# Kernel optimization log

Hardware: AMD Instinct MI355X
Metric: run time of the kernel (lower is better)

The kernel has to match this reference:

```python
import jax, jax.numpy as jnp
import numpy as np

REST = 0.0
DECAY = 0.2
THRESHOLD = 0.3
BETA = 0.02
SG_WIDTH = 1.0  # rectangular surrogate-gradient window width


@jax.custom_vjp
def spike(v, thresh):
    # forward: hard threshold, y = (v > thresh)
    return (v > thresh).astype(v.dtype)


def _spike_fwd(v, thresh):
    return spike(v, thresh), (v, thresh)


def _spike_bwd(res, g):
    v, thresh = res
    # rectangular surrogate gradient w.r.t. v; threshold gets the negative
    sg = (jnp.abs(v - thresh) < (SG_WIDTH * 0.5)).astype(g.dtype) / SG_WIDTH
    gv = g * sg
    return (gv, -gv)


spike.defvjp(_spike_fwd, _spike_bwd)


def setup_inputs() -> dict:
    key = jax.random.key(0)
    k1, k2 = jax.random.split(key)
    T, B, N = 512, 64, 1024
    tx = jax.random.normal(k1, (T, B, N), dtype=jnp.float32)
    TE = jax.random.normal(k2, (N, T), dtype=jnp.float32) * 0.1  # learned temporal encoding
    return {"tx": tx, "TE": TE}


def reference(tx, TE):
    # tx: [T, B, N] time-major input; TE: [N, T] per-neuron temporal encoding
    T, B, N = tx.shape
    v0 = jnp.full((B, N), REST, tx.dtype)
    y0 = jnp.zeros((B, N), tx.dtype)
    th0 = jnp.full((B, N), THRESHOLD, tx.dtype)

    def step(carry, inp):
        v, y, th = carry
        x, te_t = inp  # x: [B, N], te_t: [N]
        th = th + v * te_t - (th - THRESHOLD) * BETA
        v = v * DECAY * (1.0 - y) + x
        y = spike(v, th)
        return (v, y, th), y

    _, ty = jax.lax.scan(step, (v0, y0, th0), (tx, TE.T))
    return ty  # [T, B, N] spike trains
```

## Files before the change

kernel.cpp:

```cpp
#include <hip/hip_runtime.h>


#define T_STEPS 512
#define BN      (64 * 1024)

#define NTL(i)  __builtin_nontemporal_load(txp + (size_t)(i) * BN)
#define LD4(i)  (*reinterpret_cast<const float4*>(tep + (i)))

#define PFX(r, base) \
  r##0 .x = NTL((base)+0);  r##0 .y = NTL((base)+1);  r##0 .z = NTL((base)+2);  r##0 .w = NTL((base)+3);  \
  r##1 .x = NTL((base)+4);  r##1 .y = NTL((base)+5);  r##1 .z = NTL((base)+6);  r##1 .w = NTL((base)+7);  \
  r##2 .x = NTL((base)+8);  r##2 .y = NTL((base)+9);  r##2 .z = NTL((base)+10); r##2 .w = NTL((base)+11); \
  r##3 .x = NTL((base)+12); r##3 .y = NTL((base)+13); r##3 .z = NTL((base)+14); r##3 .w = NTL((base)+15);

#define PFE(r, base) \
  r##0 = LD4((base)+0); r##1 = LD4((base)+4); r##2 = LD4((base)+8); r##3 = LD4((base)+12);

#define STEP1(xv, tv, tt) { \
  float A_ = v * (tv); float B_ = th + A_; float C_ = th - 0.3f; \
  float D_ = C_ * 0.02f; th = B_ - D_; \
  float E_ = v * 0.2f; float F_ = 1.0f - y; float G_ = E_ * F_; \
  v = G_ + (xv); y = (v > th) ? 1.0f : 0.0f; \
  __builtin_nontemporal_store(y, outp + (size_t)(tt) * BN); }

#define COMP(r, s, base) \
  STEP1(r##0 .x, s##0 .x, (base)+0)  STEP1(r##0 .y, s##0 .y, (base)+1)  \
  STEP1(r##0 .z, s##0 .z, (base)+2)  STEP1(r##0 .w, s##0 .w, (base)+3)  \
  STEP1(r##1 .x, s##1 .x, (base)+4)  STEP1(r##1 .y, s##1 .y, (base)+5)  \
  STEP1(r##1 .z, s##1 .z, (base)+6)  STEP1(r##1 .w, s##1 .w, (base)+7)  \
  STEP1(r##2 .x, s##2 .x, (base)+8)  STEP1(r##2 .y, s##2 .y, (base)+9)  \
  STEP1(r##2 .z, s##2 .z, (base)+10) STEP1(r##2 .w, s##2 .w, (base)+11) \
  STEP1(r##3 .x, s##3 .x, (base)+12) STEP1(r##3 .y, s##3 .y, (base)+13) \
  STEP1(r##3 .z, s##3 .z, (base)+14) STEP1(r##3 .w, s##3 .w, (base)+15)

#define PIN() __builtin_amdgcn_sched_barrier(0)

__global__ __launch_bounds__(256, 1) void telif_kernel(
    const float* __restrict__ tx, const float* __restrict__ TE,
    float* __restrict__ out)
{
#pragma clang fp contract(off)

    const int flat = blockIdx.x * 256 + threadIdx.x;
    const int n = flat & 1023;

    const float* txp  = tx + flat;
    const float* tep  = TE + n * T_STEPS;
    float*       outp = out + flat;

    float v = 0.0f, y = 0.0f, th = 0.3f;

    float4 a0, a1, a2, a3, e0, e1, e2, e3;
    float4 b0, b1, b2, b3, f0, f1, f2, f3;
    float4 c0, c1, c2, c3, g0, g1, g2, g3;
    float4 d0, d1, d2, d3, h0, h1, h2, h3;

    PFX(a, 0)  PFE(e, 0)
    PFX(b, 16) PFE(f, 16)
    PIN();

#pragma unroll 1
    for (int t = 0; t < 448; t += 64) {
        PFX(c, t + 32) PFE(g, t + 32)
        PFX(d, t + 48) PFE(h, t + 48)
        PIN();
        COMP(a, e, t)
        COMP(b, f, t + 16)
        PIN();
        PFX(a, t + 64) PFE(e, t + 64)
        PFX(b, t + 80) PFE(f, t + 80)
        PIN();
        COMP(c, g, t + 32)
        COMP(d, h, t + 48)
        PIN();
    }
    PFX(c, 480) PFE(g, 480)
    PFX(d, 496) PFE(h, 496)
    PIN();
    COMP(a, e, 448)
    COMP(b, f, 464)
    COMP(c, g, 480)
    COMP(d, h, 496)
}

extern "C" void kernel_launch(void* const* d_in, const int* in_sizes, int n_in,
                              void* d_out, int out_size, void* d_ws, size_t ws_size,
                              hipStream_t stream) {
    const float* tx = (const float*)d_in[0];
    const float* TE = (const float*)d_in[1];
    float* out = (float*)d_out;
    telif_kernel<<<BN / 256, 256, 0, stream>>>(tx, TE, out);
}
```

Before: 233.6 us.

## Process two neurons per thread with 64-bit vector loads and smaller blocks

Result: no change. 235.5 us (+0.8%).

```diff
diff --git a/kernel.cpp b/kernel.cpp
--- a/kernel.cpp
+++ b/kernel.cpp
@@ -4,56 +4,71 @@
 #define T_STEPS 512
 #define BN      (64 * 1024)
 
-#define NTL(i)  __builtin_nontemporal_load(txp + (size_t)(i) * BN)
-#define LD4(i)  (*reinterpret_cast<const float4*>(tep + (i)))
+typedef float v2f __attribute__((ext_vector_type(2)));
+typedef float v4f __attribute__((ext_vector_type(4)));
+
+#define NTL2(i) __builtin_nontemporal_load(reinterpret_cast<const v2f*>(txp + (size_t)(i) * BN))
+#define LDA(i)  (*reinterpret_cast<const v4f*>(tep0 + (i)))
+#define LDB(i)  (*reinterpret_cast<const v4f*>(tep1 + (i)))
+
+#define DECLC(r, s) \
+  v2f r##00, r##01, r##02, r##03, r##04, r##05, r##06, r##07, \
+      r##08, r##09, r##10, r##11, r##12, r##13, r##14, r##15; \
+  v4f s##0, s##1, s##2, s##3, s##4, s##5, s##6, s##7;
 
 #define PFX(r, base) \
-  r##0 .x = NTL((base)+0);  r##0 .y = NTL((base)+1);  r##0 .z = NTL((base)+2);  r##0 .w = NTL((base)+3);  \
-  r##1 .x = NTL((base)+4);  r##1 .y = NTL((base)+5);  r##1 .z = NTL((base)+6);  r##1 .w = NTL((base)+7);  \
-  r##2 .x = NTL((base)+8);  r##2 .y = NTL((base)+9);  r##2 .z = NTL((base)+10); r##2 .w = NTL((base)+11); \
-  r##3 .x = NTL((base)+12); r##3 .y = NTL((base)+13); r##3 .z = NTL((base)+14); r##3 .w = NTL((base)+15);
+  r##00 = NTL2((base)+0);  r##01 = NTL2((base)+1);  r##02 = NTL2((base)+2);  r##03 = NTL2((base)+3);  \
+  r##04 = NTL2((base)+4);  r##05 = NTL2((base)+5);  r##06 = NTL2((base)+6);  r##07 = NTL2((base)+7);  \
+  r##08 = NTL2((base)+8);  r##09 = NTL2((base)+9);  r##10 = NTL2((base)+10); r##11 = NTL2((base)+11); \
+  r##12 = NTL2((base)+12); r##13 = NTL2((base)+13); r##14 = NTL2((base)+14); r##15 = NTL2((base)+15);
 
-#define PFE(r, base) \
-  r##0 = LD4((base)+0); r##1 = LD4((base)+4); r##2 = LD4((base)+8); r##3 = LD4((base)+12);
+#define PFE(s, base) \
+  s##0 = LDA((base));    s##1 = LDA((base)+4);  s##2 = LDA((base)+8);  s##3 = LDA((base)+12); \
+  s##4 = LDB((base));    s##5 = LDB((base)+4);  s##6 = LDB((base)+8);  s##7 = LDB((base)+12);
 
-#define STEP1(xv, tv, tt) { \
-  float A_ = v * (tv); float B_ = th + A_; float C_ = th - 0.3f; \
-  float D_ = C_ * 0.02f; th = B_ - D_; \
-  float E_ = v * 0.2f; float F_ = 1.0f - y; float G_ = E_ * F_; \
-  v = G_ + (xv); y = (v > th) ? 1.0f : 0.0f; \
-  __builtin_nontemporal_store(y, outp + (size_t)(tt) * BN); }
+#define STEP2(xv, t0v, t1v, tt) { \
+  float A0_ = v0 * (t0v); float B0_ = th0 + A0_; float C0_ = th0 - 0.3f; \
+  float D0_ = C0_ * 0.02f; th0 = B0_ - D0_; \
+  float E0_ = v0 * 0.2f; float F0_ = 1.0f - y0; float G0_ = E0_ * F0_; \
+  v0 = G0_ + (xv).x; y0 = (v0 > th0) ? 1.0f : 0.0f; \
+  float A1_ = v1 * (t1v); float B1_ = th1 + A1_; float C1_ = th1 - 0.3f; \
+  float D1_ = C1_ * 0.02f; th1 = B1_ - D1_; \
+  float E1_ = v1 * 0.2f; float F1_ = 1.0f - y1; float G1_ = E1_ * F1_; \
+  v1 = G1_ + (xv).y; y1 = (v1 > th1) ? 1.0f : 0.0f; \
+  v2f Y_; Y_.x = y0; Y_.y = y1; \
+  __builtin_nontemporal_store(Y_, reinterpret_cast<v2f*>(outp + (size_t)(tt) * BN)); }
 
 #define COMP(r, s, base) \
-  STEP1(r##0 .x, s##0 .x, (base)+0)  STEP1(r##0 .y, s##0 .y, (base)+1)  \
-  STEP1(r##0 .z, s##0 .z, (base)+2)  STEP1(r##0 .w, s##0 .w, (base)+3)  \
-  STEP1(r##1 .x, s##1 .x, (base)+4)  STEP1(r##1 .y, s##1 .y, (base)+5)  \
-  STEP1(r##1 .z, s##1 .z, (base)+6)  STEP1(r##1 .w, s##1 .w, (base)+7)  \
-  STEP1(r##2 .x, s##2 .x, (base)+8)  STEP1(r##2 .y, s##2 .y, (base)+9)  \
-  STEP1(r##2 .z, s##2 .z, (base)+10) STEP1(r##2 .w, s##2 .w, (base)+11) \
-  STEP1(r##3 .x, s##3 .x, (base)+12) STEP1(r##3 .y, s##3 .y, (base)+13) \
-  STEP1(r##3 .z, s##3 .z, (base)+14) STEP1(r##3 .w, s##3 .w, (base)+15)
+  STEP2(r##00, s##0 .x, s##4 .x, (base)+0)  STEP2(r##01, s##0 .y, s##4 .y, (base)+1)  \
+  STEP2(r##02, s##0 .z, s##4 .z, (base)+2)  STEP2(r##03, s##0 .w, s##4 .w, (base)+3)  \
+  STEP2(r##04, s##1 .x, s##5 .x, (base)+4)  STEP2(r##05, s##1 .y, s##5 .y, (base)+5)  \
+  STEP2(r##06, s##1 .z, s##5 .z, (base)+6)  STEP2(r##07, s##1 .w, s##5 .w, (base)+7)  \
+  STEP2(r##08, s##2 .x, s##6 .x, (base)+8)  STEP2(r##09, s##2 .y, s##6 .y, (base)+9)  \
+  STEP2(r##10, s##2 .z, s##6 .z, (base)+10) STEP2(r##11, s##2 .w, s##6 .w, (base)+11) \
+  STEP2(r##12, s##3 .x, s##7 .x, (base)+12) STEP2(r##13, s##3 .y, s##7 .y, (base)+13) \
+  STEP2(r##14, s##3 .z, s##7 .z, (base)+14) STEP2(r##15, s##3 .w, s##7 .w, (base)+15)
 
 #define PIN() __builtin_amdgcn_sched_barrier(0)
 
-__global__ __launch_bounds__(256, 1) void telif_kernel(
+__global__ __launch_bounds__(64, 1) void telif_kernel(
     const float* __restrict__ tx, const float* __restrict__ TE,
     float* __restrict__ out)
 {
 #pragma clang fp contract(off)
 
-    const int flat = blockIdx.x * 256 + threadIdx.x;
-    const int n = flat & 1023;
+    const int gid   = blockIdx.x * 64 + threadIdx.x;
+    const int flat2 = gid * 2;
+    const int n     = flat2 & 1023;
 
-    const float* txp  = tx + flat;
-    const float* tep  = TE + n * T_STEPS;
-    float*       outp = out + flat;
+    const float* txp  = tx + flat2;
+    const float* tep0 = TE + n * T_STEPS;
+    const float* tep1 = tep0 + T_STEPS;
+    float*       outp = out + flat2;
 
-    float v = 0.0f, y = 0.0f, th = 0.3f;
+    float v0 = 0.0f, y0 = 0.0f, th0 = 0.3f;
+    float v1 = 0.0f, y1 = 0.0f, th1 = 0.3f;
 
-    float4 a0, a1, a2, a3, e0, e1, e2, e3;
-    float4 b0, b1, b2, b3, f0, f1, f2, f3;
-    float4 c0, c1, c2, c3, g0, g1, g2, g3;
-    float4 d0, d1, d2, d3, h0, h1, h2, h3;
+    DECLC(a, e) DECLC(b, f) DECLC(c, g) DECLC(d, h)
 
     PFX(a, 0)  PFE(e, 0)
     PFX(b, 16) PFE(f, 16)
@@ -89,5 +104,5 @@
     const float* tx = (const float*)d_in[0];
     const float* TE = (const float*)d_in[1];
     float* out = (float*)d_out;
-    telif_kernel<<<BN / 256, 256, 0, stream>>>(tx, TE, out);
+    telif_kernel<<<512, 64, 0, stream>>>(tx, TE, out);
 }
```
